# Performance work log

Measured on AMD Instinct MI355X. Metric: run time of the kernel, lower is better.

The kernel has to match this reference:

```python
import jax, jax.numpy as jnp
import numpy as np

N_HEAD = 16
N_KV = 4
HEAD_DIM = 128
WINDOW = 1024
SINK = 4
THETA = 10000.0


def _rope_cos_sin(T, dim, theta, dtype):
    inv_freq = 1.0 / (theta ** (jnp.arange(0, dim, 2, dtype=jnp.float32) / dim))
    t = jnp.arange(T, dtype=jnp.float32)
    ang = jnp.outer(t, inv_freq)  # [T, dim/2]
    return jnp.cos(ang).astype(dtype), jnp.sin(ang).astype(dtype)


def _apply_rope(x, cos, sin):
    # x: [B, H, T, D]; cos/sin: [T, D/2]
    d2 = x.shape[-1] // 2
    x1, x2 = x[..., :d2], x[..., d2:]
    return jnp.concatenate([x1 * cos - x2 * sin, x2 * cos + x1 * sin], axis=-1)


def setup_inputs() -> dict:
    key = jax.random.key(0)
    ks = jax.random.split(key, 5)
    B, T, C = 2, 2048, 2048
    x = jax.random.normal(ks[0], (B, T, C), dtype=jnp.float32)
    s = 0.02
    wq = jax.random.normal(ks[1], (C, C), dtype=jnp.float32) * s
    wk = jax.random.normal(ks[2], (N_KV * HEAD_DIM, C), dtype=jnp.float32) * s
    wv = jax.random.normal(ks[3], (N_KV * HEAD_DIM, C), dtype=jnp.float32) * s
    wo = jax.random.normal(ks[4], (C, C), dtype=jnp.float32) * s
    return {"x": x, "wq": wq, "wk": wk, "wv": wv, "wo": wo}


def reference(x, wq, wk, wv, wo):
    B, T, C = x.shape
    # QKV projections (Linear with weight [out, in], no bias)
    q = (x @ wq.T).reshape(B, T, N_HEAD, HEAD_DIM).transpose(0, 2, 1, 3)  # [B,H,T,D]
    k = (x @ wk.T).reshape(B, T, N_KV, HEAD_DIM).transpose(0, 2, 1, 3)    # [B,Hkv,T,D]
    v = (x @ wv.T).reshape(B, T, N_KV, HEAD_DIM).transpose(0, 2, 1, 3)

    cos, sin = _rope_cos_sin(T, HEAD_DIM, THETA, x.dtype)
    q = _apply_rope(q, cos, sin)
    k = _apply_rope(k, cos, sin)

    # GQA: repeat kv heads to match query heads (repeat_interleave on head dim)
    rep = N_HEAD // N_KV
    k = jnp.repeat(k, rep, axis=1)
    v = jnp.repeat(v, rep, axis=1)

    # causal + sliding window + attention sink mask
    i = jnp.arange(T)[:, None]
    j = jnp.arange(T)[None, :]
    allowed = (j <= i) & (((i - j) <= WINDOW) | (j < SINK))
    bias = jnp.where(allowed, 0.0, -jnp.inf).astype(x.dtype)  # [T,T]

    scale = 1.0 / np.sqrt(HEAD_DIM)
    att = jnp.einsum("bhqd,bhkd->bhqk", q, k) * scale + bias
    att = jax.nn.softmax(att, axis=-1)
    y = jnp.einsum("bhqk,bhkd->bhqd", att, v)  # [B,H,T,D]
    y = y.transpose(0, 2, 1, 3).reshape(B, T, C)
    return y @ wo.T
```

## Files before the change

kernel.cpp:

```cpp
#include <hip/hip_runtime.h>
#include <hip/hip_bf16.h>

typedef __bf16 bf16x8 __attribute__((ext_vector_type(8)));
typedef __bf16 bf16x4 __attribute__((ext_vector_type(4)));
typedef float  f32x4  __attribute__((ext_vector_type(4)));
typedef float  f32x16 __attribute__((ext_vector_type(16)));
typedef unsigned int uint4v __attribute__((ext_vector_type(4)));

#define NB     2
#define TT     2048
#define CC     2048
#define NH     16
#define NKV    4
#define HD     128
#define WIN    1024
#define SINKN  4
#define QSCALE2 (0.08838834764831845f * 1.44269504088896340f)

__device__ __forceinline__ void lds_load16(const void* g, void* l) {
    __builtin_amdgcn_global_load_lds(
        (__attribute__((address_space(1))) void*)const_cast<void*>(g),
        (__attribute__((address_space(3))) void*)l, 16, 0, 0);
}

__device__ __forceinline__ unsigned pack2bf(float a, float b) {
    __bf16 x = (__bf16)a, y = (__bf16)b;
    unsigned short ux = __builtin_bit_cast(unsigned short, x);
    unsigned short uy = __builtin_bit_cast(unsigned short, y);
    return (unsigned)ux | ((unsigned)uy << 16);
}

__device__ __forceinline__ float fast_exp2(float x) {
    float r;
    asm("v_exp_f32 %0, %1" : "=v"(r) : "v"(x));
    return r;
}

__global__ void prolog_kernel(const float* __restrict__ x,
                              const float* __restrict__ wq, const float* __restrict__ wk,
                              const float* __restrict__ wv, const float* __restrict__ wo,
                              __bf16* __restrict__ xb, __bf16* __restrict__ Wall,
                              float* __restrict__ cosT, float* __restrict__ sinT) {
    const int g = blockIdx.x * 256 + threadIdx.x;
    if (g < 2097152) {
        const int idx = g * 4;
        const float4 v = *(const float4*)(x + idx);
        bf16x4 o;
        o[0] = (__bf16)v.x; o[1] = (__bf16)v.y; o[2] = (__bf16)v.z; o[3] = (__bf16)v.w;
        *(bf16x4*)(xb + idx) = o;
    } else if (g < 4718592) {
        const int idx = (g - 2097152) * 4;
        const float* src; int off;
        if (idx < 4194304)      { src = wq; off = idx; }
        else if (idx < 5242880) { src = wk; off = idx - 4194304; }
        else if (idx < 6291456) { src = wv; off = idx - 5242880; }
        else                    { src = wo; off = idx - 6291456; }
        const float4 v = *(const float4*)(src + off);
        bf16x4 o;
        o[0] = (__bf16)v.x; o[1] = (__bf16)v.y; o[2] = (__bf16)v.z; o[3] = (__bf16)v.w;
        *(bf16x4*)(Wall + idx) = o;
    } else {
        const int i = g - 4718592;
        const int t = i >> 6, d = i & 63;
        const float inv_freq = 1.0f / powf(10000.0f, (float)d * (1.0f / 64.0f));
        const float ang = (float)t * inv_freq;
        cosT[i] = cosf(ang);
        sinT[i] = sinf(ang);
    }
}

__global__ void scatter_vt_kernel(const __bf16* __restrict__ qkv,
                                  const float* __restrict__ cosT,
                                  const float* __restrict__ sinT,
                                  __bf16* __restrict__ Qo,
                                  __bf16* __restrict__ Ko,
                                  __bf16* __restrict__ Vt) {
    __shared__ __bf16 tile[64][72];
    if (blockIdx.x < 2560) {
        const int job = blockIdx.x * 256 + threadIdx.x;
        int m, d8, base_off; __bf16* outp; float scale;
        if (job < 524288) {
            m = job >> 7;
            const int pj = job & 127;
            const int hh = pj >> 3; d8 = pj & 7;
            base_off = hh * 128;
            const int b = m >> 11, t = m & 2047;
            outp = Qo + ((size_t)(b * NH + hh) * TT + t) * HD + d8 * 8;
            scale = QSCALE2;
        } else {
            const int j2 = job - 524288;
            m = j2 >> 5;
            const int pj = j2 & 31;
            const int g = pj >> 3; d8 = pj & 7;
            base_off = 2048 + g * 128;
            const int b = m >> 11, t = m & 2047;
            outp = Ko + ((size_t)(b * NKV + g) * TT + t) * HD + d8 * 8;
            scale = 1.0f;
        }
        const int t = m & 2047;
        const __bf16* row = qkv + (size_t)m * 3072 + base_off + d8 * 8;
        const bf16x8 x1 = *(const bf16x8*)row;
        const bf16x8 x2 = *(const bf16x8*)(row + 64);
        const float4 c0 = *(const float4*)(cosT + t * 64 + d8 * 8);
        const float4 c1 = *(const float4*)(cosT + t * 64 + d8 * 8 + 4);
        const float4 s0 = *(const float4*)(sinT + t * 64 + d8 * 8);
        const float4 s1 = *(const float4*)(sinT + t * 64 + d8 * 8 + 4);
        const float cs[8] = {c0.x, c0.y, c0.z, c0.w, c1.x, c1.y, c1.z, c1.w};
        const float sn[8] = {s0.x, s0.y, s0.z, s0.w, s1.x, s1.y, s1.z, s1.w};
        bf16x8 o1, o2;
#pragma unroll
        for (int e = 0; e < 8; ++e) {
            const float a = (float)x1[e], bb = (float)x2[e];
            o1[e] = (__bf16)((a * cs[e] - bb * sn[e]) * scale);
            o2[e] = (__bf16)((bb * cs[e] + a * sn[e]) * scale);
        }
        *(bf16x8*)outp = o1;
        *(bf16x8*)(outp + 64) = o2;
    } else {
        const int idx2 = blockIdx.x - 2560;
        const int t0 = (idx2 & 31) << 6, d0 = ((idx2 >> 5) & 1) << 6, bkv = idx2 >> 6;
        const int b = bkv >> 2, g = bkv & 3;
        const int r = threadIdx.x >> 2, cg = threadIdx.x & 3;
        const __bf16* src = qkv + (size_t)(b * TT + t0 + r) * 3072 + 2560 + g * 128 + d0 + cg * 16;
        *(bf16x8*)&tile[r][cg * 16]     = *(const bf16x8*)src;
        *(bf16x8*)&tile[r][cg * 16 + 8] = *(const bf16x8*)(src + 8);
        __syncthreads();
        __bf16* dst = Vt + ((size_t)bkv * HD + d0 + r) * TT + t0 + cg * 16;
        bf16x8 o0, o1;
#pragma unroll
        for (int c2 = 0; c2 < 8; ++c2) {
            o0[c2] = tile[cg * 16 + c2][r];
            o1[c2] = tile[cg * 16 + 8 + c2][r];
        }
        *(bf16x8*)dst = o0;
        *(bf16x8*)(dst + 8) = o1;
    }
}

template <int OUT_BF16>
__global__ __launch_bounds__(512, 2) void gemm_bt8(const __bf16* __restrict__ A,
                                                   const __bf16* __restrict__ Bm,
                                                   void* __restrict__ C,
                                                   int M, int N, int K) {
    __shared__ __align__(16) __bf16 lA[2][256 * 64];
    __shared__ __align__(16) __bf16 lB[2][256 * 64];
    const int tid = threadIdx.x;
    const int lane = tid & 63;
    const int w = tid >> 6;
    const int wm = w >> 2, wn = w & 3;
    const int nbn = N >> 8;
    const int nwg = (M >> 8) * nbn;
    const int chunk = nwg >> 3;
    const int swz = (blockIdx.x & 7) * chunk + (blockIdx.x >> 3);
    const int bm = swz / nbn, bn = swz % nbn;
    const int m0 = bm << 8, n0 = bn << 8;
    const int lr = lane & 15, lh = lane >> 4;
    const int NT = K >> 6;

    auto stageA = [&](int kt, int buf, int i) {
        const int d = i * 8192 + tid * 16;
        const int row = d >> 7;
        const int colb = (d & 127) ^ ((row & 7) << 4);
        lds_load16(A + (size_t)(m0 + row) * K + kt * 64 + (colb >> 1),
                   (char*)lA[buf] + i * 8192 + w * 1024);
    };
    auto stageB = [&](int kt, int buf, int i) {
        const int d = i * 8192 + tid * 16;
        const int row = d >> 7;
        const int colb = (d & 127) ^ ((row & 7) << 4);
        lds_load16(Bm + (size_t)(n0 + row) * K + kt * 64 + (colb >> 1),
                   (char*)lB[buf] + i * 8192 + w * 1024);
    };

    f32x4 acc[8][4] = {};

#pragma unroll
    for (int i = 0; i < 4; ++i) stageA(0, 0, i);
#pragma unroll
    for (int i = 0; i < 4; ++i) stageB(0, 0, i);
    asm volatile("s_waitcnt vmcnt(0)" ::: "memory");
    __syncthreads();

    for (int kt = 0; kt < NT; ++kt) {
        const int cur = kt & 1, nxt = cur ^ 1;
        const bool pf = (kt + 1 < NT);
        const char* bA = (const char*)lA[cur];
        const char* bB = (const char*)lB[cur];

        bf16x8 aF[4][2], b0[2][2], b1[2][2];
#pragma unroll
        for (int mf = 0; mf < 4; ++mf)
#pragma unroll
            for (int ks = 0; ks < 2; ++ks) {
                const int row = wm * 128 + mf * 16 + lr;
                const int cb = (ks * 64 + lh * 16) ^ ((row & 7) << 4);
                aF[mf][ks] = *(const bf16x8*)(bA + row * 128 + cb);
            }
#pragma unroll
        for (int nf = 0; nf < 2; ++nf)
#pragma unroll
            for (int ks = 0; ks < 2; ++ks) {
                const int row = wn * 64 + nf * 16 + lr;
                const int cb = (ks * 64 + lh * 16) ^ ((row & 7) << 4);
                b0[nf][ks] = *(const bf16x8*)(bB + row * 128 + cb);
            }
        if (pf) { stageA(kt + 1, nxt, 0); stageA(kt + 1, nxt, 1); stageA(kt + 1, nxt, 2); stageA(kt + 1, nxt, 3); }
        __builtin_amdgcn_s_setprio(1);
#pragma unroll
        for (int mf = 0; mf < 4; ++mf)
#pragma unroll
            for (int nf = 0; nf < 2; ++nf)
#pragma unroll
                for (int ks = 0; ks < 2; ++ks)
                    acc[mf][nf] = __builtin_amdgcn_mfma_f32_16x16x32_bf16(aF[mf][ks], b0[nf][ks], acc[mf][nf], 0, 0, 0);
        __builtin_amdgcn_s_setprio(0);

#pragma unroll
        for (int nf = 0; nf < 2; ++nf)
#pragma unroll
            for (int ks = 0; ks < 2; ++ks) {
                const int row = wn * 64 + 32 + nf * 16 + lr;
                const int cb = (ks * 64 + lh * 16) ^ ((row & 7) << 4);
                b1[nf][ks] = *(const bf16x8*)(bB + row * 128 + cb);
            }
        if (pf) { stageB(kt + 1, nxt, 0); stageB(kt + 1, nxt, 1); stageB(kt + 1, nxt, 2); stageB(kt + 1, nxt, 3); }
        __builtin_amdgcn_s_setprio(1);
#pragma unroll
        for (int mf = 0; mf < 4; ++mf)
#pragma unroll
            for (int nf = 0; nf < 2; ++nf)
#pragma unroll
                for (int ks = 0; ks < 2; ++ks)
                    acc[mf][nf + 2] = __builtin_amdgcn_mfma_f32_16x16x32_bf16(aF[mf][ks], b1[nf][ks], acc[mf][nf + 2], 0, 0, 0);
        __builtin_amdgcn_s_setprio(0);

#pragma unroll
        for (int mf = 0; mf < 4; ++mf)
#pragma unroll
            for (int ks = 0; ks < 2; ++ks) {
                const int row = wm * 128 + 64 + mf * 16 + lr;
                const int cb = (ks * 64 + lh * 16) ^ ((row & 7) << 4);
                aF[mf][ks] = *(const bf16x8*)(bA + row * 128 + cb);
            }
        __builtin_amdgcn_s_setprio(1);
#pragma unroll
        for (int mf = 0; mf < 4; ++mf)
#pragma unroll
            for (int nf = 0; nf < 2; ++nf)
#pragma unroll
                for (int ks = 0; ks < 2; ++ks)
                    acc[mf + 4][nf] = __builtin_amdgcn_mfma_f32_16x16x32_bf16(aF[mf][ks], b0[nf][ks], acc[mf + 4][nf], 0, 0, 0);
        __builtin_amdgcn_s_setprio(0);

        __builtin_amdgcn_s_setprio(1);
#pragma unroll
        for (int mf = 0; mf < 4; ++mf)
#pragma unroll
            for (int nf = 0; nf < 2; ++nf)
#pragma unroll
                for (int ks = 0; ks < 2; ++ks)
                    acc[mf + 4][nf + 2] = __builtin_amdgcn_mfma_f32_16x16x32_bf16(aF[mf][ks], b1[nf][ks], acc[mf + 4][nf + 2], 0, 0, 0);
        __builtin_amdgcn_s_setprio(0);

        asm volatile("s_waitcnt vmcnt(0)" ::: "memory");
        __syncthreads();
    }

#pragma unroll
    for (int mf = 0; mf < 8; ++mf)
#pragma unroll
        for (int nf = 0; nf < 4; ++nf)
#pragma unroll
            for (int r = 0; r < 4; ++r) {
                const size_t row = m0 + wm * 128 + mf * 16 + lh * 4 + r;
                const size_t col = n0 + wn * 64 + nf * 16 + lr;
                if (OUT_BF16) ((__bf16*)C)[row * N + col] = (__bf16)acc[mf][nf][r];
                else          ((float*)C)[row * N + col]  = acc[mf][nf][r];
            }
}

template <int OUT_BF16>
__global__ __launch_bounds__(256, 2) void gemm_bt(const __bf16* __restrict__ A,
                                                  const __bf16* __restrict__ Bm,
                                                  void* __restrict__ C,
                                                  int M, int N, int K) {
    __shared__ __align__(16) __bf16 lA[2][128 * 64];
    __shared__ __align__(16) __bf16 lB[2][128 * 64];
    const int tid = threadIdx.x;
    const int lane = tid & 63;
    const int w = tid >> 6;
    const int wr = w >> 1, wc = w & 1;
    const int nbn = N >> 7;
    const int nwg = (M >> 7) * nbn;
    const int chunk = nwg >> 3;
    const int swz = (blockIdx.x & 7) * chunk + (blockIdx.x >> 3);
    const int bm = swz / nbn, bn = swz % nbn;
    const int m0 = bm << 7, n0 = bn << 7;
    const int lr = lane & 15, lh = lane >> 4;
    f32x4 acc[4][4] = {};

    auto stage = [&](int k0, int buf) {
#pragma unroll
        for (int i = 0; i < 4; ++i) {
            const int d = i * 4096 + tid * 16;
            const int row = d >> 7;
            const int colb = (d & 127) ^ ((row & 7) << 4);
            lds_load16(A + (size_t)(m0 + row) * K + k0 + (colb >> 1),
                       (char*)lA[buf] + i * 4096 + w * 1024);
            lds_load16(Bm + (size_t)(n0 + row) * K + k0 + (colb >> 1),
                       (char*)lB[buf] + i * 4096 + w * 1024);
        }
    };

    stage(0, 0);
    asm volatile("s_waitcnt vmcnt(0)" ::: "memory");
    __syncthreads();

    const int NT = K >> 6;
    for (int kt = 0; kt < NT; ++kt) {
        const int buf = kt & 1;
        if (kt + 1 < NT) stage((kt + 1) << 6, buf ^ 1);

        const char* bA = (const char*)lA[buf];
        const char* bB = (const char*)lB[buf];
        bf16x8 af[4][2], bfr[4][2];
#pragma unroll
        for (int t = 0; t < 4; ++t)
#pragma unroll
            for (int ks = 0; ks < 2; ++ks) {
                const int rowa = wr * 64 + t * 16 + lr;
                const int cba = (ks * 64 + lh * 16) ^ ((rowa & 7) << 4);
                af[t][ks] = *(const bf16x8*)(bA + rowa * 128 + cba);
                const int rowb = wc * 64 + t * 16 + lr;
                const int cbb = (ks * 64 + lh * 16) ^ ((rowb & 7) << 4);
                bfr[t][ks] = *(const bf16x8*)(bB + rowb * 128 + cbb);
            }
#pragma unroll
        for (int mt = 0; mt < 4; ++mt)
#pragma unroll
            for (int nt = 0; nt < 4; ++nt)
#pragma unroll
                for (int ks = 0; ks < 2; ++ks)
                    acc[mt][nt] = __builtin_amdgcn_mfma_f32_16x16x32_bf16(af[mt][ks], bfr[nt][ks], acc[mt][nt], 0, 0, 0);

        asm volatile("s_waitcnt vmcnt(0)" ::: "memory");
        __syncthreads();
    }

    const int r0 = (lane >> 4) * 4;
#pragma unroll
    for (int mt = 0; mt < 4; ++mt)
#pragma unroll
        for (int nt = 0; nt < 4; ++nt)
#pragma unroll
            for (int r = 0; r < 4; ++r) {
                const size_t row = m0 + wr * 64 + mt * 16 + r0 + r;
                const size_t col = n0 + wc * 64 + nt * 16 + lr;
                if (OUT_BF16) ((__bf16*)C)[row * N + col] = (__bf16)acc[mt][nt][r];
                else          ((float*)C)[row * N + col]  = acc[mt][nt][r];
            }
}

__global__ __launch_bounds__(256, 2) void attn_kernel(const __bf16* __restrict__ Q,
                                                      const __bf16* __restrict__ Kg,
                                                      const __bf16* __restrict__ Vt,
                                                      __bf16* __restrict__ Y) {
    const int id = blockIdx.x;
    const int grp = id & 7;
    const int pos = id >> 3;
    const int kv = grp & 3, b = grp >> 2;
    const int qt2 = 63 - pos;
    const int q0 = qt2 << 5;
    const int tid = threadIdx.x, lane = tid & 63, w = tid >> 6;
    const int l31 = lane & 31, hi = lane >> 5;
    const int h  = kv * 4 + w;

    __shared__ __align__(16) __bf16 lK[64 * 128];
    __shared__ __align__(16) __bf16 lV[128 * 64];

    bf16x8 qf[8];
    {
        const __bf16* Qb = Q + ((size_t)(b * NH + h) * TT + q0) * HD;
#pragma unroll
        for (int c = 0; c < 8; ++c)
            qf[c] = *(const bf16x8*)(Qb + l31 * HD + c * 16 + hi * 8);
    }

    f32x16 acc[4] = {};
    float mrun = -1e30f, lrun = 0.f;
    const int iq = q0 + l31;

    const __bf16* Kb = Kg + (size_t)(b * NKV + kv) * TT * HD;
    const __bf16* Vb = Vt + (size_t)(b * NKV + kv) * HD * TT;
    const int jend = qt2 >> 1;
    const int jsw  = (q0 > WIN) ? ((q0 - WIN) >> 6) : 0;

    for (int jb = 0; jb <= jend; ++jb) {
        if (jb > 0 && jb < jsw) continue;
        const int j0 = jb << 6;
        __syncthreads();
#pragma unroll
        for (int i = 0; i < 4; ++i) {
            const int o = i * 4096 + tid * 16;
            {
                const int row = o >> 8;
                const int colb = (o & 255) ^ ((row & 7) << 4);
                lds_load16(Kb + (size_t)(j0 + row) * HD + (colb >> 1),
                           (char*)lK + i * 4096 + w * 1024);
            }
            {
                const int row = o >> 7;
                const int colb = (o & 127) ^ ((row & 7) << 4);
                lds_load16(Vb + (size_t)row * TT + j0 + (colb >> 1),
                           (char*)lV + i * 4096 + w * 1024);
            }
        }
        asm volatile("s_waitcnt vmcnt(0)" ::: "memory");
        __syncthreads();

        f32x16 st[2];
#pragma unroll
        for (int kt2 = 0; kt2 < 2; ++kt2) {
            f32x16 s = {};
#pragma unroll
            for (int c = 0; c < 8; ++c) {
                const int row = kt2 * 32 + l31;
                const int cb = (c * 32 + hi * 16) ^ ((row & 7) << 4);
                const bf16x8 kf = *(const bf16x8*)((const char*)lK + row * 256 + cb);
                s = __builtin_amdgcn_mfma_f32_32x32x16_bf16(kf, qf[c], s, 0, 0, 0);
            }
            st[kt2] = s;
        }

        const bool fullTile = (j0 + 63 <= q0) && (q0 + 31 - j0 <= WIN);
        if (!fullTile) {
#pragma unroll
            for (int kt2 = 0; kt2 < 2; ++kt2)
#pragma unroll
                for (int rr = 0; rr < 16; ++rr) {
                    const int j = j0 + kt2 * 32 + (rr & 3) + 8 * (rr >> 2) + 4 * hi;
                    const bool ok = (j <= iq) && ((iq - j <= WIN) || (j < SINKN));
                    if (!ok) st[kt2][rr] = -1e30f;
                }
        }

        float mx = st[0][0];
#pragma unroll
        for (int kt2 = 0; kt2 < 2; ++kt2)
#pragma unroll
            for (int rr = 0; rr < 16; ++rr) mx = fmaxf(mx, st[kt2][rr]);
        mx = fmaxf(mx, __shfl_xor(mx, 32, 64));

        if (!__all(mx - mrun <= 11.53f)) {
            const float mnew = fmaxf(mrun, mx);
            const float corr = fast_exp2(mrun - mnew);
            mrun = mnew;
            lrun *= corr;
#pragma unroll
            for (int rr = 0; rr < 16; ++rr) {
                const float cq = __shfl(corr, (rr & 3) + 8 * (rr >> 2) + 4 * hi, 64);
#pragma unroll
                for (int dt = 0; dt < 4; ++dt) acc[dt][rr] *= cq;
            }
        }

        float rsum = 0.f;
#pragma unroll
        for (int kt2 = 0; kt2 < 2; ++kt2)
#pragma unroll
            for (int rr = 0; rr < 16; ++rr) {
                const float p = fast_exp2(st[kt2][rr] - mrun);
                st[kt2][rr] = p;
                rsum += p;
            }
        rsum += __shfl_xor(rsum, 32, 64);
        lrun += rsum;

        bf16x8 pa[4];
#pragma unroll
        for (int c = 0; c < 4; ++c) {
            const int kt2 = c >> 1, g = c & 1, base = 8 * g;
            const unsigned u1a = pack2bf(st[kt2][base + 0], st[kt2][base + 1]);
            const unsigned u1b = pack2bf(st[kt2][base + 2], st[kt2][base + 3]);
            const unsigned u2a = pack2bf(st[kt2][base + 4], st[kt2][base + 5]);
            const unsigned u2b = pack2bf(st[kt2][base + 6], st[kt2][base + 7]);
            const unsigned p1a = (unsigned)__shfl_xor((int)u1a, 32, 64);
            const unsigned p1b = (unsigned)__shfl_xor((int)u1b, 32, 64);
            const unsigned p2a = (unsigned)__shfl_xor((int)u2a, 32, 64);
            const unsigned p2b = (unsigned)__shfl_xor((int)u2b, 32, 64);
            uint4v uv;
            uv[0] = hi ? p2a : u1a;
            uv[1] = hi ? p2b : u1b;
            uv[2] = hi ? u2a : p1a;
            uv[3] = hi ? u2b : p1b;
            pa[c] = __builtin_bit_cast(bf16x8, uv);
        }

#pragma unroll
        for (int dt = 0; dt < 4; ++dt) {
            const int row = dt * 32 + l31;
            const int swzr = (row & 7) << 4;
#pragma unroll
            for (int c = 0; c < 4; ++c) {
                const int cb = (c * 32 + hi * 16) ^ swzr;
                const bf16x8 vf = *(const bf16x8*)((const char*)lV + row * 128 + cb);
                acc[dt] = __builtin_amdgcn_mfma_f32_32x32x16_bf16(pa[c], vf, acc[dt], 0, 0, 0);
            }
        }
    }

    const float inv = 1.f / lrun;
    float invq[16];
#pragma unroll
    for (int rr = 0; rr < 16; ++rr)
        invq[rr] = __shfl(inv, (rr & 3) + 8 * (rr >> 2) + 4 * hi, 64);
#pragma unroll
    for (int dt = 0; dt < 4; ++dt)
#pragma unroll
        for (int rr = 0; rr < 16; ++rr) {
            const int qrow = (rr & 3) + 8 * (rr >> 2) + 4 * hi;
            Y[((size_t)b * TT + q0 + qrow) * CC + h * HD + dt * 32 + l31] =
                (__bf16)(acc[dt][rr] * invq[rr]);
        }
}

extern "C" void kernel_launch(void* const* d_in, const int* in_sizes, int n_in,
                              void* d_out, int out_size, void* d_ws, size_t ws_size,
                              hipStream_t stream) {
    const float* x  = (const float*)d_in[0];
    const float* wq = (const float*)d_in[1];
    const float* wk = (const float*)d_in[2];
    const float* wv = (const float*)d_in[3];
    const float* wo = (const float*)d_in[4];
    float* out = (float*)d_out;

    char* ws = (char*)d_ws;
    size_t off = 0;
    auto alloc = [&](size_t bytes) { char* p = ws + off; off += bytes; return p; };
    __bf16* xb   = (__bf16*)alloc(16777216);
    __bf16* Wall = (__bf16*)alloc(12582912);
    __bf16* wob  = (__bf16*)alloc(8388608);
    __bf16* qkv  = (__bf16*)alloc(25165824);
    __bf16* Qs   = (__bf16*)alloc(16777216);
    __bf16* Ks   = (__bf16*)alloc(4194304);
    __bf16* Vts  = (__bf16*)alloc(4194304);
    float*  cosT = (float*)alloc(524288);
    float*  sinT = (float*)alloc(524288);
    __bf16* Yb = xb;

    prolog_kernel<<<18944, 256, 0, stream>>>(x, wq, wk, wv, wo, xb, Wall, cosT, sinT);
    gemm_bt8<1><<<dim3(16 * 12), 512, 0, stream>>>(xb, Wall, qkv, 4096, 3072, 2048);
    scatter_vt_kernel<<<3072, 256, 0, stream>>>(qkv, cosT, sinT, Qs, Ks, Vts);
    attn_kernel<<<dim3(512), 256, 0, stream>>>(Qs, Ks, Vts, Yb);
    gemm_bt<0><<<dim3(32 * 16), 256, 0, stream>>>(Yb, wob, out, 4096, 2048, 2048);
}
```

Before: 160.5 us.

## Split attention KV range across two wave groups with split-K softmax merge

Doubles the attention block to 512 threads so each head gets two waves that process alternating KV tiles from two LDS buffers. The partial max, sum and accumulators are then merged through LDS at the end. This adds parallelism and occupancy for the few 512-block attention grid, and halves the number of serial KV iterations per wave. In exchange it needs more registers per wave under launch_bounds(512,4), twice the LDS, and an extra merge phase with several barriers.

```diff
diff --git a/kernel.cpp b/kernel.cpp
--- a/kernel.cpp
+++ b/kernel.cpp
@@ -361,7 +361,7 @@
             }
 }
 
-__global__ __launch_bounds__(256, 2) void attn_kernel(const __bf16* __restrict__ Q,
+__global__ __launch_bounds__(512, 4) void attn_kernel(const __bf16* __restrict__ Q,
                                                       const __bf16* __restrict__ Kg,
                                                       const __bf16* __restrict__ Vt,
                                                       __bf16* __restrict__ Y) {
@@ -373,10 +373,11 @@
     const int q0 = qt2 << 5;
     const int tid = threadIdx.x, lane = tid & 63, w = tid >> 6;
     const int l31 = lane & 31, hi = lane >> 5;
-    const int h  = kv * 4 + w;
-
-    __shared__ __align__(16) __bf16 lK[64 * 128];
-    __shared__ __align__(16) __bf16 lV[128 * 64];
+    const int hh = w >> 1, ss = w & 1;
+    const int h  = kv * 4 + hh;
+
+    __shared__ __align__(16) __bf16 lK[2][64 * 128];
+    __shared__ __align__(16) __bf16 lV[2][128 * 64];
 
     bf16x8 qf[8];
     {
@@ -394,134 +395,189 @@
     const __bf16* Vb = Vt + (size_t)(b * NKV + kv) * HD * TT;
     const int jend = qt2 >> 1;
     const int jsw  = (q0 > WIN) ? ((q0 - WIN) >> 6) : 0;
-
-    for (int jb = 0; jb <= jend; ++jb) {
-        if (jb > 0 && jb < jsw) continue;
-        const int j0 = jb << 6;
-        __syncthreads();
-#pragma unroll
-        for (int i = 0; i < 4; ++i) {
-            const int o = i * 4096 + tid * 16;
+    const int jswe = (jsw < 1) ? 1 : jsw;
+    const int nv   = (jend >= jswe) ? (jend - jswe + 2) : 1;
+
+    auto stage = [&](int jb, int buf) {
+        const int j0s = jb << 6;
+#pragma unroll
+        for (int L = 0; L < 2; ++L) {
+            const int o = L * 8192 + w * 1024 + lane * 16;
             {
                 const int row = o >> 8;
                 const int colb = (o & 255) ^ ((row & 7) << 4);
-                lds_load16(Kb + (size_t)(j0 + row) * HD + (colb >> 1),
-                           (char*)lK + i * 4096 + w * 1024);
+                lds_load16(Kb + (size_t)(j0s + row) * HD + (colb >> 1),
+                           (char*)lK[buf] + L * 8192 + w * 1024);
             }
             {
                 const int row = o >> 7;
                 const int colb = (o & 127) ^ ((row & 7) << 4);
-                lds_load16(Vb + (size_t)row * TT + j0 + (colb >> 1),
-                           (char*)lV + i * 4096 + w * 1024);
-            }
+                lds_load16(Vb + (size_t)row * TT + j0s + (colb >> 1),
+                           (char*)lV[buf] + L * 8192 + w * 1024);
+            }
+        }
+    };
+
+    for (int i = 0;; ++i) {
+        const int base = 2 * i;
+        if (base >= nv) break;
+        __syncthreads();
+        {
+            const int jb0 = (base == 0) ? 0 : (jswe + base - 1);
+            stage(jb0, 0);
+            if (base + 1 < nv) stage(jswe + base, 1);
         }
         asm volatile("s_waitcnt vmcnt(0)" ::: "memory");
         __syncthreads();
 
-        f32x16 st[2];
-#pragma unroll
-        for (int kt2 = 0; kt2 < 2; ++kt2) {
-            f32x16 s = {};
-#pragma unroll
-            for (int c = 0; c < 8; ++c) {
-                const int row = kt2 * 32 + l31;
-                const int cb = (c * 32 + hi * 16) ^ ((row & 7) << 4);
-                const bf16x8 kf = *(const bf16x8*)((const char*)lK + row * 256 + cb);
-                s = __builtin_amdgcn_mfma_f32_32x32x16_bf16(kf, qf[c], s, 0, 0, 0);
-            }
-            st[kt2] = s;
-        }
-
-        const bool fullTile = (j0 + 63 <= q0) && (q0 + 31 - j0 <= WIN);
-        if (!fullTile) {
+        const int myidx = base + ss;
+        if (myidx < nv) {
+            const int jb = (myidx == 0) ? 0 : (jswe + myidx - 1);
+            const int j0 = jb << 6;
+            const char* bK = (const char*)lK[ss];
+            const char* bV = (const char*)lV[ss];
+
+            f32x16 st[2];
+#pragma unroll
+            for (int kt2 = 0; kt2 < 2; ++kt2) {
+                f32x16 s = {};
+#pragma unroll
+                for (int c = 0; c < 8; ++c) {
+                    const int row = kt2 * 32 + l31;
+                    const int cb = (c * 32 + hi * 16) ^ ((row & 7) << 4);
+                    const bf16x8 kf = *(const bf16x8*)(bK + row * 256 + cb);
+                    s = __builtin_amdgcn_mfma_f32_32x32x16_bf16(kf, qf[c], s, 0, 0, 0);
+                }
+                st[kt2] = s;
+            }
+
+            const bool fullTile = (j0 + 63 <= q0) && (q0 + 31 - j0 <= WIN);
+            if (!fullTile) {
+#pragma unroll
+                for (int kt2 = 0; kt2 < 2; ++kt2)
+#pragma unroll
+                    for (int rr = 0; rr < 16; ++rr) {
+                        const int j = j0 + kt2 * 32 + (rr & 3) + 8 * (rr >> 2) + 4 * hi;
+                        const bool ok = (j <= iq) && ((iq - j <= WIN) || (j < SINKN));
+                        if (!ok) st[kt2][rr] = -1e30f;
+                    }
+            }
+
+            float mx = st[0][0];
 #pragma unroll
             for (int kt2 = 0; kt2 < 2; ++kt2)
 #pragma unroll
+                for (int rr = 0; rr < 16; ++rr) mx = fmaxf(mx, st[kt2][rr]);
+            mx = fmaxf(mx, __shfl_xor(mx, 32, 64));
+
+            if (!__all(mx - mrun <= 11.53f)) {
+                const float mnew = fmaxf(mrun, mx);
+                const float corr = fast_exp2(mrun - mnew);
+                mrun = mnew;
+                lrun *= corr;
+#pragma unroll
                 for (int rr = 0; rr < 16; ++rr) {
-                    const int j = j0 + kt2 * 32 + (rr & 3) + 8 * (rr >> 2) + 4 * hi;
-                    const bool ok = (j <= iq) && ((iq - j <= WIN) || (j < SINKN));
-                    if (!ok) st[kt2][rr] = -1e30f;
+                    const float cq = __shfl(corr, (rr & 3) + 8 * (rr >> 2) + 4 * hi, 64);
+#pragma unroll
+                    for (int dt = 0; dt < 4; ++dt) acc[dt][rr] *= cq;
                 }
-        }
-
-        float mx = st[0][0];
-#pragma unroll
-        for (int kt2 = 0; kt2 < 2; ++kt2)
-#pragma unroll
-            for (int rr = 0; rr < 16; ++rr) mx = fmaxf(mx, st[kt2][rr]);
-        mx = fmaxf(mx, __shfl_xor(mx, 32, 64));
-
-        if (!__all(mx - mrun <= 11.53f)) {
-            const float mnew = fmaxf(mrun, mx);
-            const float corr = fast_exp2(mrun - mnew);
-            mrun = mnew;
-            lrun *= corr;
+            }
+
+            float rsum = 0.f;
+#pragma unroll
+            for (int kt2 = 0; kt2 < 2; ++kt2)
+#pragma unroll
+                for (int rr = 0; rr < 16; ++rr) {
+                    const float p = fast_exp2(st[kt2][rr] - mrun);
+                    st[kt2][rr] = p;
+                    rsum += p;
+                }
+            rsum += __shfl_xor(rsum, 32, 64);
+            lrun += rsum;
+
+            bf16x8 pa[4];
+#pragma unroll
+            for (int c = 0; c < 4; ++c) {
+                const int kt2 = c >> 1, g = c & 1, base2 = 8 * g;
+                const unsigned u1a = pack2bf(st[kt2][base2 + 0], st[kt2][base2 + 1]);
+                const unsigned u1b = pack2bf(st[kt2][base2 + 2], st[kt2][base2 + 3]);
+                const unsigned u2a = pack2bf(st[kt2][base2 + 4], st[kt2][base2 + 5]);
+                const unsigned u2b = pack2bf(st[kt2][base2 + 6], st[kt2][base2 + 7]);
+                const unsigned p1a = (unsigned)__shfl_xor((int)u1a, 32, 64);
+                const unsigned p1b = (unsigned)__shfl_xor((int)u1b, 32, 64);
+                const unsigned p2a = (unsigned)__shfl_xor((int)u2a, 32, 64);
+                const unsigned p2b = (unsigned)__shfl_xor((int)u2b, 32, 64);
+                uint4v uv;
+                uv[0] = hi ? p2a : u1a;
+                uv[1] = hi ? p2b : u1b;
+                uv[2] = hi ? u2a : p1a;
+                uv[3] = hi ? u2b : p1b;
+                pa[c] = __builtin_bit_cast(bf16x8, uv);
+            }
+
+#pragma unroll
+            for (int dt = 0; dt < 4; ++dt) {
+                const int row = dt * 32 + l31;
+                const int swzr = (row & 7) << 4;
+#pragma unroll
+                for (int c = 0; c < 4; ++c) {
+                    const int cb = (c * 32 + hi * 16) ^ swzr;
+                    const bf16x8 vf = *(const bf16x8*)(bV + row * 128 + cb);
+                    acc[dt] = __builtin_amdgcn_mfma_f32_32x32x16_bf16(pa[c], vf, acc[dt], 0, 0, 0);
+                }
+            }
+        }
+    }
+
+    float* mlbuf  = (float*)lV;
+    float* accbuf = (float*)lK;
+    __syncthreads();
+    if (ss == 1) {
+        mlbuf[(hh * 64 + lane) * 2 + 0] = mrun;
+        mlbuf[(hh * 64 + lane) * 2 + 1] = lrun;
+    }
+    __syncthreads();
+    float c0 = 1.f, c1 = 0.f;
+    if (ss == 0) {
+        const float m1 = mlbuf[(hh * 64 + lane) * 2 + 0];
+        const float l1 = mlbuf[(hh * 64 + lane) * 2 + 1];
+        const float mtot = fmaxf(mrun, m1);
+        c0 = fast_exp2(mrun - mtot);
+        c1 = fast_exp2(m1 - mtot);
+        lrun = lrun * c0 + l1 * c1;
+    }
+#pragma unroll
+    for (int dt = 0; dt < 4; ++dt) {
+        __syncthreads();
+        if (ss == 1) {
+#pragma unroll
+            for (int rr = 0; rr < 16; ++rr)
+                accbuf[(hh * 64 + lane) * 16 + rr] = acc[dt][rr];
+        }
+        __syncthreads();
+        if (ss == 0) {
 #pragma unroll
             for (int rr = 0; rr < 16; ++rr) {
-                const float cq = __shfl(corr, (rr & 3) + 8 * (rr >> 2) + 4 * hi, 64);
-#pragma unroll
-                for (int dt = 0; dt < 4; ++dt) acc[dt][rr] *= cq;
-            }
-        }
-
-        float rsum = 0.f;
-#pragma unroll
-        for (int kt2 = 0; kt2 < 2; ++kt2)
+                const int qrow = (rr & 3) + 8 * (rr >> 2) + 4 * hi;
+                const float c0q = __shfl(c0, qrow, 64);
+                const float c1q = __shfl(c1, qrow, 64);
+                acc[dt][rr] = acc[dt][rr] * c0q + accbuf[(hh * 64 + lane) * 16 + rr] * c1q;
+            }
+        }
+    }
+
+    if (ss == 0) {
+        const float inv = 1.f / lrun;
+#pragma unroll
+        for (int dt = 0; dt < 4; ++dt)
 #pragma unroll
             for (int rr = 0; rr < 16; ++rr) {
-                const float p = fast_exp2(st[kt2][rr] - mrun);
-                st[kt2][rr] = p;
-                rsum += p;
-            }
-        rsum += __shfl_xor(rsum, 32, 64);
-        lrun += rsum;
-
-        bf16x8 pa[4];
-#pragma unroll
-        for (int c = 0; c < 4; ++c) {
-            const int kt2 = c >> 1, g = c & 1, base = 8 * g;
-            const unsigned u1a = pack2bf(st[kt2][base + 0], st[kt2][base + 1]);
-            const unsigned u1b = pack2bf(st[kt2][base + 2], st[kt2][base + 3]);
-            const unsigned u2a = pack2bf(st[kt2][base + 4], st[kt2][base + 5]);
-            const unsigned u2b = pack2bf(st[kt2][base + 6], st[kt2][base + 7]);
-            const unsigned p1a = (unsigned)__shfl_xor((int)u1a, 32, 64);
-            const unsigned p1b = (unsigned)__shfl_xor((int)u1b, 32, 64);
-            const unsigned p2a = (unsigned)__shfl_xor((int)u2a, 32, 64);
-            const unsigned p2b = (unsigned)__shfl_xor((int)u2b, 32, 64);
-            uint4v uv;
-            uv[0] = hi ? p2a : u1a;
-            uv[1] = hi ? p2b : u1b;
-            uv[2] = hi ? u2a : p1a;
-            uv[3] = hi ? u2b : p1b;
-            pa[c] = __builtin_bit_cast(bf16x8, uv);
-        }
-
-#pragma unroll
-        for (int dt = 0; dt < 4; ++dt) {
-            const int row = dt * 32 + l31;
-            const int swzr = (row & 7) << 4;
-#pragma unroll
-            for (int c = 0; c < 4; ++c) {
-                const int cb = (c * 32 + hi * 16) ^ swzr;
-                const bf16x8 vf = *(const bf16x8*)((const char*)lV + row * 128 + cb);
-                acc[dt] = __builtin_amdgcn_mfma_f32_32x32x16_bf16(pa[c], vf, acc[dt], 0, 0, 0);
-            }
-        }
-    }
-
-    const float inv = 1.f / lrun;
-    float invq[16];
-#pragma unroll
-    for (int rr = 0; rr < 16; ++rr)
-        invq[rr] = __shfl(inv, (rr & 3) + 8 * (rr >> 2) + 4 * hi, 64);
-#pragma unroll
-    for (int dt = 0; dt < 4; ++dt)
-#pragma unroll
-        for (int rr = 0; rr < 16; ++rr) {
-            const int qrow = (rr & 3) + 8 * (rr >> 2) + 4 * hi;
-            Y[((size_t)b * TT + q0 + qrow) * CC + h * HD + dt * 32 + l31] =
-                (__bf16)(acc[dt][rr] * invq[rr]);
-        }
+                const int qrow = (rr & 3) + 8 * (rr >> 2) + 4 * hi;
+                const float invq = __shfl(inv, qrow, 64);
+                Y[((size_t)b * TT + q0 + qrow) * CC + h * HD + dt * 32 + l31] =
+                    (__bf16)(acc[dt][rr] * invq);
+            }
+    }
 }
 
 extern "C" void kernel_launch(void* const* d_in, const int* in_sizes, int n_in,
@@ -551,6 +607,6 @@
     prolog_kernel<<<18944, 256, 0, stream>>>(x, wq, wk, wv, wo, xb, Wall, cosT, sinT);
     gemm_bt8<1><<<dim3(16 * 12), 512, 0, stream>>>(xb, Wall, qkv, 4096, 3072, 2048);
     scatter_vt_kernel<<<3072, 256, 0, stream>>>(qkv, cosT, sinT, Qs, Ks, Vts);
-    attn_kernel<<<dim3(512), 256, 0, stream>>>(Qs, Ks, Vts, Yb);
+    attn_kernel<<<dim3(512), 512, 0, stream>>>(Qs, Ks, Vts, Yb);
     gemm_bt<0><<<dim3(32 * 16), 256, 0, stream>>>(Yb, wob, out, 4096, 2048, 2048);
 }
```

Measured after the change: 300.1 us. 87.0% more time.
